# Kernel optimization log

Hardware: AMD Instinct MI355X
Metric: run time of the kernel (lower is better)

The kernel has to match this reference:

```python
import jax, jax.numpy as jnp
import numpy as np

N, K, C, J = 200000, 512, 64, 32  # nodes, node feature dim, mixture components (Ccurr+1), macrostates


def setup_inputs() -> dict:
    key = jax.random.key(0)
    k0, k1, k2, k3, k4, k5 = jax.random.split(key, 6)
    x = jax.random.normal(k0, (N, K), dtype=jnp.float32)
    macrostate = jax.random.randint(k1, (N,), 0, J)  # macrostate_assignments (int, constant)
    # Gaussian emission parameters theta[k] (diagonal covariance), one per component
    mu = jax.random.normal(k2, (C, K), dtype=jnp.float32)
    log_var = 0.1 * jax.random.normal(k3, (C, K), dtype=jnp.float32)
    # stick-breaking weights beta (positive, sums to 1) and CRF counts njk (non-negative)
    b = jax.random.uniform(k4, (C,), dtype=jnp.float32) + 1e-3
    beta = b / b.sum()
    njk = 100.0 * jax.random.uniform(k5, (J, C), dtype=jnp.float32)
    alpha = jnp.float32(1.0)
    return {"x": x, "mu": mu, "log_var": log_var, "beta": beta, "njk": njk,
            "alpha": alpha, "macrostate": macrostate}


def reference(x, mu, log_var, beta, njk, alpha, macrostate):
    # f_X_theta_log[u, k] = theta[k].get_data_log_likelihood(x[u])  (diagonal Gaussian)
    # expand ||(x - mu)/sigma||^2 as a GEMM to stay compute-bound:
    inv_var = jnp.exp(-log_var)                                   # [C, K]
    quad = ((x * x) @ inv_var.T                                   # [N, C]
            - 2.0 * (x @ (mu * inv_var).T)
            + jnp.sum(mu * mu * inv_var, axis=1))
    log_norm = jnp.sum(log_var, axis=1) + x.shape[1] * jnp.log(2.0 * jnp.pi)
    f_log = -0.5 * (quad + log_norm)                              # [N, C]
    # per-node: unnorm_log_p_zu = log(alpha*beta + njk[j]) + f_X_theta_log[u]
    prior_log = jnp.log(alpha * beta[None, :] + njk)              # [J, C]
    logits = prior_log[macrostate] + f_log                        # [N, C]
    # p_zu via numerically-stable softmax; posterior_matrix[u] += p_zu
    posterior = jax.nn.softmax(logits, axis=1)
    return posterior
```

## Files before the change

### kernel.cpp

```cpp
#include <hip/hip_runtime.h>
#include <hip/hip_bf16.h>

typedef _Float16 f16;
typedef _Float16 f16x8 __attribute__((ext_vector_type(8)));
typedef float f32x4 __attribute__((ext_vector_type(4)));

#define NN 200000
#define KK 512
#define CC 64
#define JJ 32
#define WFRAG_ELEMS (48 * 4 * 64 * 8)

__global__ __launch_bounds__(256) void fill_w(const float* __restrict__ mu,
                                              const float* __restrict__ lv,
                                              f16* __restrict__ wfrag) {
  int idx = blockIdx.x * 256 + threadIdx.x;
  int i = idx & 7, l = (idx >> 3) & 63, ct = (idx >> 9) & 3, kF = idx >> 11;
  int k = (kF & 15) * 32 + (l >> 4) * 8 + i;
  int c = ct * 16 + (l & 15);
  int sec = kF >> 4;
  float lvv = lv[c * KK + k];
  float w;
  if (sec == 0) {
    w = -0.5f * expm1f(-lvv);
  } else {
    float w2 = mu[c * KK + k] * expf(-lvv);
    float wh = (float)(f16)w2;
    w = (sec == 1) ? wh : (w2 - wh);
  }
  wfrag[idx] = (f16)w;
}

__global__ __launch_bounds__(64) void fill_bias(const float* __restrict__ mu,
                                                const float* __restrict__ lv,
                                                const float* __restrict__ beta,
                                                const float* __restrict__ njk,
                                                const float* __restrict__ alphap,
                                                float* __restrict__ bias) {
  int c = blockIdx.x;
  int lane = threadIdx.x;
  float s = 0.0f;
  for (int k = lane; k < KK; k += 64) {
    float l2 = lv[c * KK + k];
    float m = mu[c * KK + k];
    s += fmaf(m * m, expf(-l2), l2);
  }
  #pragma unroll
  for (int d = 1; d < 64; d <<= 1) s += __shfl_xor(s, d, 64);
  float base = -0.5f * (s + 512.0f * 1.8378770664093453f);
  if (lane < JJ)
    bias[lane * CC + c] = logf(alphap[0] * beta[c] + njk[lane * CC + c]) + base;
}

__global__ __launch_bounds__(256, 4) void gmm_main(
    const float* __restrict__ x, const int* __restrict__ ms,
    const f16* __restrict__ wfrag, const float* __restrict__ bias,
    float* __restrict__ out) {
  const int lane = threadIdx.x & 63;
  const int wv = threadIdx.x >> 6;
  const int lr = lane & 15;
  const int kg = lane >> 4;
  const int row0 = blockIdx.x * 128 + wv * 32;
  if (row0 >= NN) return;

  f32x4 acc[2][4];
  #pragma unroll
  for (int rt = 0; rt < 2; ++rt)
    #pragma unroll
    for (int ct = 0; ct < 4; ++ct) acc[rt][ct] = (f32x4)0.0f;

  const float* xp0 = x + (size_t)(row0 + lr) * KK + kg * 8;
  const float* xp1 = xp0 + (size_t)16 * KK;
  const f16* wb = wfrag + lane * 8;

  f32x4 cx[4];
  cx[0] = __builtin_nontemporal_load(reinterpret_cast<const f32x4*>(xp0));
  cx[1] = __builtin_nontemporal_load(reinterpret_cast<const f32x4*>(xp0 + 4));
  cx[2] = __builtin_nontemporal_load(reinterpret_cast<const f32x4*>(xp1));
  cx[3] = __builtin_nontemporal_load(reinterpret_cast<const f32x4*>(xp1 + 4));

  #pragma unroll 1
  for (int s = 0; s < 16; ++s) {
    f32x4 nx[4];
    if (s < 15) {
      const float* p0 = xp0 + (s + 1) * 32;
      const float* p1 = xp1 + (s + 1) * 32;
      nx[0] = __builtin_nontemporal_load(reinterpret_cast<const f32x4*>(p0));
      nx[1] = __builtin_nontemporal_load(reinterpret_cast<const f32x4*>(p0 + 4));
      nx[2] = __builtin_nontemporal_load(reinterpret_cast<const f32x4*>(p1));
      nx[3] = __builtin_nontemporal_load(reinterpret_cast<const f32x4*>(p1 + 4));
    }

    f16x8 fxx[2], fxh[2], fxl[2];
    #pragma unroll
    for (int rt = 0; rt < 2; ++rt) {
      #pragma unroll
      for (int i = 0; i < 8; ++i) {
        float v = (i < 4) ? cx[rt * 2][i] : cx[rt * 2 + 1][i - 4];
        f16 h = (f16)v;
        fxh[rt][i] = h;
        fxl[rt][i] = (f16)(v - (float)h);
        fxx[rt][i] = (f16)(v * v);
      }
    }

    const f16* wbs = wb + (size_t)s * 2048;
    #pragma unroll
    for (int ct = 0; ct < 4; ++ct) {
      f16x8 bw1 = *reinterpret_cast<const f16x8*>(wbs + ct * 512);
      f16x8 bwh = *reinterpret_cast<const f16x8*>(wbs + 32768 + ct * 512);
      f16x8 bwl = *reinterpret_cast<const f16x8*>(wbs + 65536 + ct * 512);
      #pragma unroll
      for (int rt = 0; rt < 2; ++rt) {
        acc[rt][ct] = __builtin_amdgcn_mfma_f32_16x16x32_f16(fxx[rt], bw1, acc[rt][ct], 0, 0, 0);
        acc[rt][ct] = __builtin_amdgcn_mfma_f32_16x16x32_f16(fxh[rt], bwh, acc[rt][ct], 0, 0, 0);
        acc[rt][ct] = __builtin_amdgcn_mfma_f32_16x16x32_f16(fxh[rt], bwl, acc[rt][ct], 0, 0, 0);
        acc[rt][ct] = __builtin_amdgcn_mfma_f32_16x16x32_f16(fxl[rt], bwh, acc[rt][ct], 0, 0, 0);
      }
    }

    if (s < 15) {
      cx[0] = nx[0]; cx[1] = nx[1]; cx[2] = nx[2]; cx[3] = nx[3];
    }
  }

  #pragma unroll
  for (int rt = 0; rt < 2; ++rt) {
    int rbase = row0 + rt * 16 + kg * 4;
    #pragma unroll
    for (int r = 0; r < 4; ++r) {
      int j = ms[rbase + r];
      const float* bj = bias + j * CC + lr;
      float v0 = acc[rt][0][r] + bj[0];
      float v1 = acc[rt][1][r] + bj[16];
      float v2 = acc[rt][2][r] + bj[32];
      float v3 = acc[rt][3][r] + bj[48];
      float m = fmaxf(fmaxf(v0, v1), fmaxf(v2, v3));
      #pragma unroll
      for (int d = 1; d < 16; d <<= 1) m = fmaxf(m, __shfl_xor(m, d, 64));
      float e0 = __expf(v0 - m), e1 = __expf(v1 - m);
      float e2 = __expf(v2 - m), e3 = __expf(v3 - m);
      float sum = (e0 + e1) + (e2 + e3);
      #pragma unroll
      for (int d = 1; d < 16; d <<= 1) sum += __shfl_xor(sum, d, 64);
      float inv = 1.0f / sum;
      float* o = out + (size_t)(rbase + r) * CC + lr;
      __builtin_nontemporal_store(e0 * inv, o);
      __builtin_nontemporal_store(e1 * inv, o + 16);
      __builtin_nontemporal_store(e2 * inv, o + 32);
      __builtin_nontemporal_store(e3 * inv, o + 48);
    }
  }
}

extern "C" void kernel_launch(void* const* d_in, const int* in_sizes, int n_in,
                              void* d_out, int out_size, void* d_ws, size_t ws_size,
                              hipStream_t stream) {
  const float* x     = (const float*)d_in[0];
  const float* mu    = (const float*)d_in[1];
  const float* lv    = (const float*)d_in[2];
  const float* beta  = (const float*)d_in[3];
  const float* njk   = (const float*)d_in[4];
  const float* alpha = (const float*)d_in[5];
  const int*   ms    = (const int*)d_in[6];
  float* out = (float*)d_out;

  f16* wfrag  = (f16*)d_ws;
  float* bias = (float*)((char*)d_ws + WFRAG_ELEMS * sizeof(f16));

  fill_w<<<WFRAG_ELEMS / 256, 256, 0, stream>>>(mu, lv, wfrag);
  fill_bias<<<CC, 64, 0, stream>>>(mu, lv, beta, njk, alpha, bias);
  gmm_main<<<(NN + 127) / 128, 256, 0, stream>>>(x, ms, wfrag, bias, out);
}
```

Before: 158.8 us.

## Stage weight fragments in double-buffered LDS via direct global-to-LDS loads

Each K-step's weight fragments (three f16 sections) are now loaded cooperatively into a double-buffered shared memory tile using global_load_lds, one step ahead of use. The MFMA operands are then read from LDS instead of every wave fetching them from global/L2. This adds two block barriers per step and lowers the occupancy hint from 4 to 3 blocks per CU. Out-of-range waves now stay alive so they can take part in the barriers.

Result: faster. 129.8 us (-18.3%).

```diff
diff --git a/kernel.cpp b/kernel.cpp
--- a/kernel.cpp
+++ b/kernel.cpp
@@ -10,6 +10,12 @@
 #define CC 64
 #define JJ 32
 #define WFRAG_ELEMS (48 * 4 * 64 * 8)
+
+__device__ inline void gload_lds16(const void* g, void* l) {
+  __builtin_amdgcn_global_load_lds(
+      (const __attribute__((address_space(1))) void*)g,
+      (__attribute__((address_space(3))) void*)l, 16, 0, 0);
+}
 
 __global__ __launch_bounds__(256) void fill_w(const float* __restrict__ mu,
                                               const float* __restrict__ lv,
@@ -52,16 +58,25 @@
     bias[lane * CC + c] = logf(alphap[0] * beta[c] + njk[lane * CC + c]) + base;
 }
 
-__global__ __launch_bounds__(256, 4) void gmm_main(
+__global__ __launch_bounds__(256, 3) void gmm_main(
     const float* __restrict__ x, const int* __restrict__ ms,
     const f16* __restrict__ wfrag, const float* __restrict__ bias,
     float* __restrict__ out) {
-  const int lane = threadIdx.x & 63;
-  const int wv = threadIdx.x >> 6;
+  __shared__ char lds[2 * 12288];
+  const int t = threadIdx.x;
+  const int lane = t & 63;
+  const int wv = t >> 6;
   const int lr = lane & 15;
   const int kg = lane >> 4;
-  const int row0 = blockIdx.x * 128 + wv * 32;
-  if (row0 >= NN) return;
+  const long row0 = (long)blockIdx.x * 128 + wv * 32;
+  const bool valid = row0 < NN;
+  const long r0 = valid ? row0 + lr : 0;
+  const long r1 = valid ? row0 + 16 + lr : 0;
+
+  const float* xp0 = x + r0 * KK + kg * 8;
+  const float* xp1 = x + r1 * KK + kg * 8;
+  const char* wfb = (const char*)wfrag;
+  const int lsec = wv * 1024 + lane * 16;
 
   f32x4 acc[2][4];
   #pragma unroll
@@ -69,20 +84,27 @@
     #pragma unroll
     for (int ct = 0; ct < 4; ++ct) acc[rt][ct] = (f32x4)0.0f;
 
-  const float* xp0 = x + (size_t)(row0 + lr) * KK + kg * 8;
-  const float* xp1 = xp0 + (size_t)16 * KK;
-  const f16* wb = wfrag + lane * 8;
+  #pragma unroll
+  for (int sec = 0; sec < 3; ++sec)
+    gload_lds16(wfb + sec * 65536 + lsec, lds + sec * 4096 + wv * 1024);
 
   f32x4 cx[4];
   cx[0] = __builtin_nontemporal_load(reinterpret_cast<const f32x4*>(xp0));
   cx[1] = __builtin_nontemporal_load(reinterpret_cast<const f32x4*>(xp0 + 4));
   cx[2] = __builtin_nontemporal_load(reinterpret_cast<const f32x4*>(xp1));
   cx[3] = __builtin_nontemporal_load(reinterpret_cast<const f32x4*>(xp1 + 4));
-
+  __syncthreads();
+
+  int cur = 0;
   #pragma unroll 1
   for (int s = 0; s < 16; ++s) {
     f32x4 nx[4];
     if (s < 15) {
+      const char* gsrc = wfb + (s + 1) * 4096;
+      char* ldst = lds + (cur ^ 1) * 12288;
+      #pragma unroll
+      for (int sec = 0; sec < 3; ++sec)
+        gload_lds16(gsrc + sec * 65536 + lsec, ldst + sec * 4096 + wv * 1024);
       const float* p0 = xp0 + (s + 1) * 32;
       const float* p1 = xp1 + (s + 1) * 32;
       nx[0] = __builtin_nontemporal_load(reinterpret_cast<const f32x4*>(p0));
@@ -104,12 +126,12 @@
       }
     }
 
-    const f16* wbs = wb + (size_t)s * 2048;
+    const f16* lbase = (const f16*)(lds + cur * 12288) + lane * 8;
     #pragma unroll
     for (int ct = 0; ct < 4; ++ct) {
-      f16x8 bw1 = *reinterpret_cast<const f16x8*>(wbs + ct * 512);
-      f16x8 bwh = *reinterpret_cast<const f16x8*>(wbs + 32768 + ct * 512);
-      f16x8 bwl = *reinterpret_cast<const f16x8*>(wbs + 65536 + ct * 512);
+      f16x8 bw1 = *reinterpret_cast<const f16x8*>(lbase + ct * 512);
+      f16x8 bwh = *reinterpret_cast<const f16x8*>(lbase + 2048 + ct * 512);
+      f16x8 bwl = *reinterpret_cast<const f16x8*>(lbase + 4096 + ct * 512);
       #pragma unroll
       for (int rt = 0; rt < 2; ++rt) {
         acc[rt][ct] = __builtin_amdgcn_mfma_f32_16x16x32_f16(fxx[rt], bw1, acc[rt][ct], 0, 0, 0);
@@ -119,36 +141,40 @@
       }
     }
 
+    __syncthreads();
+    cur ^= 1;
     if (s < 15) {
       cx[0] = nx[0]; cx[1] = nx[1]; cx[2] = nx[2]; cx[3] = nx[3];
     }
   }
 
-  #pragma unroll
-  for (int rt = 0; rt < 2; ++rt) {
-    int rbase = row0 + rt * 16 + kg * 4;
-    #pragma unroll
-    for (int r = 0; r < 4; ++r) {
-      int j = ms[rbase + r];
-      const float* bj = bias + j * CC + lr;
-      float v0 = acc[rt][0][r] + bj[0];
-      float v1 = acc[rt][1][r] + bj[16];
-      float v2 = acc[rt][2][r] + bj[32];
-      float v3 = acc[rt][3][r] + bj[48];
-      float m = fmaxf(fmaxf(v0, v1), fmaxf(v2, v3));
-      #pragma unroll
-      for (int d = 1; d < 16; d <<= 1) m = fmaxf(m, __shfl_xor(m, d, 64));
-      float e0 = __expf(v0 - m), e1 = __expf(v1 - m);
-      float e2 = __expf(v2 - m), e3 = __expf(v3 - m);
-      float sum = (e0 + e1) + (e2 + e3);
-      #pragma unroll
-      for (int d = 1; d < 16; d <<= 1) sum += __shfl_xor(sum, d, 64);
-      float inv = 1.0f / sum;
-      float* o = out + (size_t)(rbase + r) * CC + lr;
-      __builtin_nontemporal_store(e0 * inv, o);
-      __builtin_nontemporal_store(e1 * inv, o + 16);
-      __builtin_nontemporal_store(e2 * inv, o + 32);
-      __builtin_nontemporal_store(e3 * inv, o + 48);
+  if (valid) {
+    #pragma unroll
+    for (int rt = 0; rt < 2; ++rt) {
+      long rbase = row0 + rt * 16 + kg * 4;
+      #pragma unroll
+      for (int r = 0; r < 4; ++r) {
+        int j = ms[rbase + r];
+        const float* bj = bias + j * CC + lr;
+        float v0 = acc[rt][0][r] + bj[0];
+        float v1 = acc[rt][1][r] + bj[16];
+        float v2 = acc[rt][2][r] + bj[32];
+        float v3 = acc[rt][3][r] + bj[48];
+        float m = fmaxf(fmaxf(v0, v1), fmaxf(v2, v3));
+        #pragma unroll
+        for (int d = 1; d < 16; d <<= 1) m = fmaxf(m, __shfl_xor(m, d, 64));
+        float e0 = __expf(v0 - m), e1 = __expf(v1 - m);
+        float e2 = __expf(v2 - m), e3 = __expf(v3 - m);
+        float sum = (e0 + e1) + (e2 + e3);
+        #pragma unroll
+        for (int d = 1; d < 16; d <<= 1) sum += __shfl_xor(sum, d, 64);
+        float inv = 1.0f / sum;
+        float* o = out + (size_t)rbase * CC + r * CC + lr;
+        __builtin_nontemporal_store(e0 * inv, o);
+        __builtin_nontemporal_store(e1 * inv, o + 16);
+        __builtin_nontemporal_store(e2 * inv, o + 32);
+        __builtin_nontemporal_store(e3 * inv, o + 48);
+      }
     }
   }
 }
```

## Use single-wave blocks with 64-row tiles to reuse weight fragments more

Applied to the files above, without the earlier changes.

Each block is now one wavefront that handles 64 rows, covered by four 16-row tiles, instead of 32 rows per wave. Each weight fragment load is therefore reused across twice as many MFMAs. The next x chunk is now loaded straight into the current registers after conversion, which removes the separate prefetch buffer. The accumulator count doubles, so register pressure rises and occupancy drops (launch bounds now 64 threads, 3 per SIMD). The bounds check is also dropped, which is safe because N is divisible by 64.

Measured after the change: 148.8 us. 6.3% less time.

```diff
diff --git a/kernel.cpp b/kernel.cpp
--- a/kernel.cpp
+++ b/kernel.cpp
@@ -10,6 +10,10 @@
 #define CC 64
 #define JJ 32
 #define WFRAG_ELEMS (48 * 4 * 64 * 8)
+
+__device__ inline f32x4 ntl(const float* p) {
+  return __builtin_nontemporal_load(reinterpret_cast<const f32x4*>(p));
+}
 
 __global__ __launch_bounds__(256) void fill_w(const float* __restrict__ mu,
                                               const float* __restrict__ lv,
@@ -52,48 +56,38 @@
     bias[lane * CC + c] = logf(alphap[0] * beta[c] + njk[lane * CC + c]) + base;
 }
 
-__global__ __launch_bounds__(256, 4) void gmm_main(
+__global__ __launch_bounds__(64, 3) void gmm_main(
     const float* __restrict__ x, const int* __restrict__ ms,
     const f16* __restrict__ wfrag, const float* __restrict__ bias,
     float* __restrict__ out) {
-  const int lane = threadIdx.x & 63;
-  const int wv = threadIdx.x >> 6;
+  const int lane = threadIdx.x;
   const int lr = lane & 15;
   const int kg = lane >> 4;
-  const int row0 = blockIdx.x * 128 + wv * 32;
-  if (row0 >= NN) return;
+  const long row0 = (long)blockIdx.x * 64;
 
-  f32x4 acc[2][4];
+  const float* xp0 = x + (row0 + 0 * 16 + lr) * KK + kg * 8;
+  const float* xp1 = x + (row0 + 1 * 16 + lr) * KK + kg * 8;
+  const float* xp2 = x + (row0 + 2 * 16 + lr) * KK + kg * 8;
+  const float* xp3 = x + (row0 + 3 * 16 + lr) * KK + kg * 8;
+  const f16* wb = wfrag + lane * 8;
+
+  f32x4 acc[4][4];
   #pragma unroll
-  for (int rt = 0; rt < 2; ++rt)
+  for (int rt = 0; rt < 4; ++rt)
     #pragma unroll
     for (int ct = 0; ct < 4; ++ct) acc[rt][ct] = (f32x4)0.0f;
 
-  const float* xp0 = x + (size_t)(row0 + lr) * KK + kg * 8;
-  const float* xp1 = xp0 + (size_t)16 * KK;
-  const f16* wb = wfrag + lane * 8;
-
-  f32x4 cx[4];
-  cx[0] = __builtin_nontemporal_load(reinterpret_cast<const f32x4*>(xp0));
-  cx[1] = __builtin_nontemporal_load(reinterpret_cast<const f32x4*>(xp0 + 4));
-  cx[2] = __builtin_nontemporal_load(reinterpret_cast<const f32x4*>(xp1));
-  cx[3] = __builtin_nontemporal_load(reinterpret_cast<const f32x4*>(xp1 + 4));
+  f32x4 cx[8];
+  cx[0] = ntl(xp0); cx[1] = ntl(xp0 + 4);
+  cx[2] = ntl(xp1); cx[3] = ntl(xp1 + 4);
+  cx[4] = ntl(xp2); cx[5] = ntl(xp2 + 4);
+  cx[6] = ntl(xp3); cx[7] = ntl(xp3 + 4);
 
   #pragma unroll 1
   for (int s = 0; s < 16; ++s) {
-    f32x4 nx[4];
-    if (s < 15) {
-      const float* p0 = xp0 + (s + 1) * 32;
-      const float* p1 = xp1 + (s + 1) * 32;
-      nx[0] = __builtin_nontemporal_load(reinterpret_cast<const f32x4*>(p0));
-      nx[1] = __builtin_nontemporal_load(reinterpret_cast<const f32x4*>(p0 + 4));
-      nx[2] = __builtin_nontemporal_load(reinterpret_cast<const f32x4*>(p1));
-      nx[3] = __builtin_nontemporal_load(reinterpret_cast<const f32x4*>(p1 + 4));
-    }
-
-    f16x8 fxx[2], fxh[2], fxl[2];
+    f16x8 fxx[4], fxh[4], fxl[4];
     #pragma unroll
-    for (int rt = 0; rt < 2; ++rt) {
+    for (int rt = 0; rt < 4; ++rt) {
       #pragma unroll
       for (int i = 0; i < 8; ++i) {
         float v = (i < 4) ? cx[rt * 2][i] : cx[rt * 2 + 1][i - 4];
@@ -103,7 +97,13 @@
         fxx[rt][i] = (f16)(v * v);
       }
     }
-
+    if (s < 15) {
+      const int o = (s + 1) * 32;
+      cx[0] = ntl(xp0 + o); cx[1] = ntl(xp0 + o + 4);
+      cx[2] = ntl(xp1 + o); cx[3] = ntl(xp1 + o + 4);
+      cx[4] = ntl(xp2 + o); cx[5] = ntl(xp2 + o + 4);
+      cx[6] = ntl(xp3 + o); cx[7] = ntl(xp3 + o + 4);
+    }
     const f16* wbs = wb + (size_t)s * 2048;
     #pragma unroll
     for (int ct = 0; ct < 4; ++ct) {
@@ -111,22 +111,18 @@
       f16x8 bwh = *reinterpret_cast<const f16x8*>(wbs + 32768 + ct * 512);
       f16x8 bwl = *reinterpret_cast<const f16x8*>(wbs + 65536 + ct * 512);
       #pragma unroll
-      for (int rt = 0; rt < 2; ++rt) {
+      for (int rt = 0; rt < 4; ++rt) {
         acc[rt][ct] = __builtin_amdgcn_mfma_f32_16x16x32_f16(fxx[rt], bw1, acc[rt][ct], 0, 0, 0);
         acc[rt][ct] = __builtin_amdgcn_mfma_f32_16x16x32_f16(fxh[rt], bwh, acc[rt][ct], 0, 0, 0);
         acc[rt][ct] = __builtin_amdgcn_mfma_f32_16x16x32_f16(fxh[rt], bwl, acc[rt][ct], 0, 0, 0);
         acc[rt][ct] = __builtin_amdgcn_mfma_f32_16x16x32_f16(fxl[rt], bwh, acc[rt][ct], 0, 0, 0);
       }
     }
-
-    if (s < 15) {
-      cx[0] = nx[0]; cx[1] = nx[1]; cx[2] = nx[2]; cx[3] = nx[3];
-    }
   }
 
   #pragma unroll
-  for (int rt = 0; rt < 2; ++rt) {
-    int rbase = row0 + rt * 16 + kg * 4;
+  for (int rt = 0; rt < 4; ++rt) {
+    long rbase = row0 + rt * 16 + kg * 4;
     #pragma unroll
     for (int r = 0; r < 4; ++r) {
       int j = ms[rbase + r];
@@ -170,5 +166,5 @@
 
   fill_w<<<WFRAG_ELEMS / 256, 256, 0, stream>>>(mu, lv, wfrag);
   fill_bias<<<CC, 64, 0, stream>>>(mu, lv, beta, njk, alpha, bias);
-  gmm_main<<<(NN + 127) / 128, 256, 0, stream>>>(x, ms, wfrag, bias, out);
+  gmm_main<<<NN / 64, 64, 0, stream>>>(x, ms, wfrag, bias, out);
 }
```
